# Kernel tuning notes

Measured on AMD Instinct MI355X. Metric: run time of the kernel, lower is better.

Reference implementation:

```python
import jax, jax.numpy as jnp
import numpy as np

NUM_HEADS = 12
HEAD_DIM = 64
EPS = 1e-6


def _layernorm(x, g, b):
    mu = jnp.mean(x, axis=-1, keepdims=True)
    var = jnp.mean(jnp.square(x - mu), axis=-1, keepdims=True)
    return (x - mu) * jax.lax.rsqrt(var + EPS) * g + b


def setup_inputs() -> dict:
    key = jax.random.key(0)
    ks = jax.random.split(key, 8)
    D, DFF = 768, 3072
    s = lambda d: 1.0 / np.sqrt(d)
    return {
        "hidden_states": jax.random.normal(ks[0], (4, 2048, D), jnp.float32),
        "ln1_g": jnp.ones((D,), jnp.float32),
        "ln1_b": jnp.zeros((D,), jnp.float32),
        "w_qkv": jax.random.normal(ks[1], (D, 3 * D), jnp.float32) * s(D),
        "b_qkv": jnp.zeros((3 * D,), jnp.float32),
        "w_attn": jax.random.normal(ks[2], (D, D), jnp.float32) * s(D),
        "b_attn": jnp.zeros((D,), jnp.float32),
        "ln2_g": jnp.ones((D,), jnp.float32),
        "ln2_b": jnp.zeros((D,), jnp.float32),
        "w_in": jax.random.normal(ks[3], (D, DFF), jnp.float32) * s(D),
        "b_in": jnp.zeros((DFF,), jnp.float32),
        "w_out": jax.random.normal(ks[4], (DFF, D), jnp.float32) * s(DFF),
        "b_out": jnp.zeros((D,), jnp.float32),
    }


def reference(hidden_states, ln1_g, ln1_b, w_qkv, b_qkv, w_attn, b_attn,
              ln2_g, ln2_b, w_in, b_in, w_out, b_out):
    B, S, D = hidden_states.shape
    residual = hidden_states
    h = _layernorm(hidden_states, ln1_g, ln1_b)
    # QKV: [B,S,3D] -> [B,S,3,H,hd] -> [3,B,H,S,hd]
    qkv = (h @ w_qkv + b_qkv).reshape(B, S, 3, NUM_HEADS, HEAD_DIM)
    qkv = jnp.transpose(qkv, (2, 0, 3, 1, 4))
    scale = HEAD_DIM ** (-0.5)
    q, k, v = qkv[0] * scale, qkv[1], qkv[2]
    scores = jnp.einsum("bhqd,bhkd->bhqk", q, k)
    attn = jax.nn.softmax(scores, axis=-1)
    o = jnp.einsum("bhqk,bhkd->bhqd", attn, v)
    o = jnp.transpose(o, (0, 2, 1, 3)).reshape(B, S, D)
    h = residual + (o @ w_attn + b_attn)
    residual2 = h
    h2 = _layernorm(h, ln2_g, ln2_b)
    h2 = jax.nn.gelu(h2 @ w_in + b_in, approximate=False)
    h2 = h2 @ w_out + b_out
    return residual2 + h2
```

## Files before the change

kernel.cpp:

```cpp
#include <hip/hip_runtime.h>

typedef __bf16 bf16_t;
typedef bf16_t bf16x8 __attribute__((ext_vector_type(8)));
typedef float f32x4 __attribute__((ext_vector_type(4)));
typedef unsigned short ushortx8 __attribute__((ext_vector_type(8)));
typedef unsigned short ushortx4 __attribute__((ext_vector_type(4)));
typedef short short4v __attribute__((ext_vector_type(4)));

union U8 { ushortx4 h[2]; bf16x8 b; ushortx8 u; };
union SV { bf16_t h[4]; short4v s; };

__device__ __forceinline__ unsigned short f2bf(float f) {
  union { bf16_t h; unsigned short u; } cv;
  cv.h = (bf16_t)f;
  return cv.u;
}

__device__ __forceinline__ void gl_lds16(const unsigned short* g, unsigned short* l) {
  __builtin_amdgcn_global_load_lds((const __attribute__((address_space(1))) void*)g,
                                   (__attribute__((address_space(3))) void*)l,
                                   16, 0, 0);
}

__device__ __forceinline__ float gelu_fast(float v) {
  float v3 = v * v * v;
  float z = -2.30211886f * v - 0.102945f * v3;
  float e = exp2f(z);
  return v * __builtin_amdgcn_rcpf(1.0f + e);
}

__global__ __launch_bounds__(256) void ln_kernel(const float* __restrict__ x,
                                                 const float* __restrict__ g,
                                                 const float* __restrict__ b,
                                                 unsigned short* __restrict__ out) {
  int row = blockIdx.x;
  int t = threadIdx.x;
  const float* xr = x + (size_t)row * 768;
  float v0 = xr[t], v1 = xr[t + 256], v2 = xr[t + 512];
  __shared__ float red[4];
  float s = v0 + v1 + v2;
  for (int o = 32; o > 0; o >>= 1) s += __shfl_down(s, o, 64);
  if ((t & 63) == 0) red[t >> 6] = s;
  __syncthreads();
  float mu = (red[0] + red[1] + red[2] + red[3]) * (1.0f / 768.0f);
  __syncthreads();
  float d0 = v0 - mu, d1 = v1 - mu, d2 = v2 - mu;
  s = d0 * d0 + d1 * d1 + d2 * d2;
  for (int o = 32; o > 0; o >>= 1) s += __shfl_down(s, o, 64);
  if ((t & 63) == 0) red[t >> 6] = s;
  __syncthreads();
  float var = (red[0] + red[1] + red[2] + red[3]) * (1.0f / 768.0f);
  float rs = rsqrtf(var + 1e-6f);
  unsigned short* orow = out + (size_t)row * 768;
  orow[t]       = f2bf(d0 * rs * g[t]       + b[t]);
  orow[t + 256] = f2bf(d1 * rs * g[t + 256] + b[t + 256]);
  orow[t + 512] = f2bf(d2 * rs * g[t + 512] + b[t + 512]);
}

__global__ __launch_bounds__(256) void transpose_all(
    const float* __restrict__ w_qkv, const float* __restrict__ w_attn,
    const float* __restrict__ w_in, const float* __restrict__ w_out,
    unsigned short* __restrict__ wqkvT, unsigned short* __restrict__ wattnT,
    unsigned short* __restrict__ winT, unsigned short* __restrict__ woutT) {
  int id = blockIdx.x;
  const float* W; unsigned short* WT; int K, N, nx, ny;
  if (id < 1728)      { W = w_qkv;  WT = wqkvT;  K = 768;  N = 2304; nx = id % 72; ny = id / 72; }
  else if (id < 2304) { id -= 1728; W = w_attn; WT = wattnT; K = 768;  N = 768;  nx = id % 24; ny = id / 24; }
  else if (id < 4608) { id -= 2304; W = w_in;   WT = winT;   K = 768;  N = 3072; nx = id % 96; ny = id / 96; }
  else                { id -= 4608; W = w_out;  WT = woutT;  K = 3072; N = 768;  nx = id % 24; ny = id / 24; }
  __shared__ float tile[32][33];
  int n0 = nx * 32, k0 = ny * 32;
  int tx = threadIdx.x, ty = threadIdx.y;
  for (int i = 0; i < 4; i++)
    tile[ty + i * 8][tx] = W[(size_t)(k0 + ty + i * 8) * N + n0 + tx];
  __syncthreads();
  for (int i = 0; i < 4; i++)
    WT[(size_t)(n0 + ty + i * 8) * K + k0 + tx] = f2bf(tile[tx][ty + i * 8]);
}

template <int EPI, int TM, int BK>
__device__ __forceinline__ void gemm_body(const unsigned short* __restrict__ A,
                                          const unsigned short* __restrict__ BT,
                                          const float* __restrict__ bias,
                                          const float* resid,
                                          void* out, unsigned short* vt, int os,
                                          int N, int K) {
  constexpr int MI = TM / 32;
  constexpr int ASZ = TM * BK;
  constexpr int BSZ = 128 * BK;
  constexpr int RP = 512 / BK;
  constexpr int NA = TM / (4 * RP);
  constexpr int NB = 128 / (4 * RP);
  constexpr int SM = BK / 8 - 1;
  __shared__ __align__(16) unsigned short smem[2 * (ASZ + BSZ)];

  int t = threadIdx.x;
  int w = t >> 6, lane = t & 63, ln = lane & 15, quad = lane >> 4;
  int wm = w & 1, wn = w >> 1;

  int gx = gridDim.x;
  int nwg = gx * gridDim.y;
  int flat = blockIdx.y * gx + blockIdx.x;
  int nf = (flat & 7) * (nwg >> 3) + (flat >> 3);
  int m0 = (nf / gx) * TM, n0 = (nf % gx) * 128;

  int lrow = lane / (BK / 8);
  int lslot = lane % (BK / 8);
  int scol = ((lslot ^ (lrow & SM)) * 8);

  const unsigned short* gA[NA];
  const unsigned short* gB[NB];
#pragma unroll
  for (int i = 0; i < NA; i++)
    gA[i] = A + (size_t)(m0 + (i * 4 + w) * RP + lrow) * K + scol;
#pragma unroll
  for (int i = 0; i < NB; i++)
    gB[i] = BT + (size_t)(n0 + (i * 4 + w) * RP + lrow) * K + scol;

  auto stage = [&](int buf) {
    unsigned short* Ab = smem + buf * ASZ;
    unsigned short* Bb = smem + 2 * ASZ + buf * BSZ;
#pragma unroll
    for (int i = 0; i < NA; i++) {
      gl_lds16(gA[i], Ab + (i * 4 + w) * 512);
      gA[i] += BK;
    }
#pragma unroll
    for (int i = 0; i < NB; i++) {
      gl_lds16(gB[i], Bb + (i * 4 + w) * 512);
      gB[i] += BK;
    }
  };

  f32x4 acc[MI][4];
  f32x4 zero = {0.f, 0.f, 0.f, 0.f};
  for (int mi = 0; mi < MI; mi++)
    for (int ni = 0; ni < 4; ni++) acc[mi][ni] = zero;

  int nk = K / BK;
  stage(0);
  int cur = 0;
  for (int kt = 0; kt < nk; kt++) {
    __syncthreads();
    if (kt + 1 < nk) stage(cur ^ 1);
    const unsigned short* Ac = smem + cur * ASZ;
    const unsigned short* Bc = smem + 2 * ASZ + cur * BSZ;
#pragma unroll
    for (int ks = 0; ks < BK / 32; ks++) {
      bf16x8 af[MI], bfr[4];
#pragma unroll
      for (int mi = 0; mi < MI; mi++) {
        int r = wm * (TM / 2) + mi * 16 + ln;
        af[mi] = *(const bf16x8*)&Ac[r * BK + (((ks * 4 + quad) ^ (r & SM)) * 8)];
      }
#pragma unroll
      for (int ni = 0; ni < 4; ni++) {
        int r = wn * 64 + ni * 16 + ln;
        bfr[ni] = *(const bf16x8*)&Bc[r * BK + (((ks * 4 + quad) ^ (r & SM)) * 8)];
      }
#pragma unroll
      for (int mi = 0; mi < MI; mi++)
#pragma unroll
        for (int ni = 0; ni < 4; ni++)
          acc[mi][ni] = __builtin_amdgcn_mfma_f32_16x16x32_bf16(af[mi], bfr[ni],
                                                                acc[mi][ni], 0, 0, 0);
    }
    cur ^= 1;
  }

  if (EPI == 2) {
    float* outp = (float*)out;
    for (int mi = 0; mi < MI; mi++) {
      for (int ni = 0; ni < 4; ni++) {
        int col = n0 + wn * 64 + ni * 16 + ln;
        float bv = bias[col];
        for (int r = 0; r < 4; r++) {
          int row = m0 + wm * (TM / 2) + mi * 16 + quad * 4 + r;
          float v = acc[mi][ni][r] + bv;
          v += resid[(size_t)row * N + col];
          outp[(size_t)row * N + col] = v;
        }
      }
    }
  } else {
    __syncthreads();
    unsigned short* Cs16 = smem + w * 1024;
    unsigned short* outp = (unsigned short*)out;
    for (int mi = 0; mi < MI; mi++) {
      for (int ni = 0; ni < 4; ni++) {
        int col = n0 + wn * 64 + ni * 16 + ln;
        float bv = bias[col];
        for (int r = 0; r < 4; r++) {
          float v = acc[mi][ni][r] + bv;
          if (EPI == 0) {
            if (col < 768) v *= 0.18033688f;
          } else {
            v = gelu_fast(v);
          }
          Cs16[(quad * 4 + r) * 64 + ni * 16 + ln] = f2bf(v);
        }
      }
      __syncthreads();
      if (EPI == 0 && n0 >= 1536) {
        int c = n0 - 1536 + wn * 64 + lane;
        int s0 = m0 + wm * (TM / 2) + mi * 16;
        int bb = s0 >> 11, sl = s0 & 2047;
        ushortx8 lo, hi;
        for (int r = 0; r < 8; r++) lo[r] = Cs16[r * 64 + lane];
        for (int r = 0; r < 8; r++) hi[r] = Cs16[(8 + r) * 64 + lane];
        size_t vbase = ((size_t)(bb * 768 + c)) * 2048 + sl;
        *(ushortx8*)&vt[vbase] = lo;
        *(ushortx8*)&vt[vbase + 8] = hi;
      } else {
        int OS = (EPI == 0) ? os : N;
        for (int j = 0; j < 2; j++) {
          int rrow = j * 8 + (lane >> 3);
          int ch = (lane & 7) * 8;
          ushortx8 pv = *(const ushortx8*)&Cs16[rrow * 64 + ch];
          *(ushortx8*)&outp[(size_t)(m0 + wm * (TM / 2) + mi * 16 + rrow) * OS +
                            n0 + wn * 64 + ch] = pv;
        }
      }
      __syncthreads();
    }
  }
}

__global__ __launch_bounds__(256) void gemm_qkv(const unsigned short* A,
    const unsigned short* BT, const float* bias, void* out, unsigned short* vt,
    int N, int K) {
  gemm_body<0, 128, 32>(A, BT, bias, nullptr, out, vt, 1536, N, K);
}
__global__ __launch_bounds__(256) void gemm_attnout(const unsigned short* A,
    const unsigned short* BT, const float* bias, const float* resid, void* out,
    int N, int K) {
  gemm_body<2, 64, 64>(A, BT, bias, resid, out, nullptr, N, N, K);
}
__global__ __launch_bounds__(256) void gemm_ffn1(const unsigned short* A,
    const unsigned short* BT, const float* bias, void* out, int N, int K) {
  gemm_body<1, 128, 32>(A, BT, bias, nullptr, out, nullptr, N, N, K);
}
__global__ __launch_bounds__(256) void gemm_ffn2(const unsigned short* A,
    const unsigned short* BT, const float* bias, const float* resid, void* out,
    int N, int K) {
  gemm_body<2, 64, 64>(A, BT, bias, resid, out, nullptr, N, N, K);
}

__global__ __launch_bounds__(512, 4) void flash_attn(
    const unsigned short* __restrict__ qk, const unsigned short* __restrict__ v_t,
    unsigned short* __restrict__ o) {
  int flat = blockIdx.y * 16 + blockIdx.x;
  int nf = (flat & 7) * 96 + (flat >> 3);
  int qt = nf % 16;
  int bh = nf / 16;
  int b = bh / 12, h = bh % 12;
  int t = threadIdx.x;
  int w = t >> 6, lane = t & 63, ln = lane & 15, quad = lane >> 4;
  int qg = w & 3, kh2 = w >> 2;

  __shared__ __align__(16) unsigned short smem[18432];
  int qrow0 = b * 2048 + qt * 128;
  int qw = qrow0 + qg * 32;

  bf16x8 qf[2][2];
  for (int qi = 0; qi < 2; qi++)
    for (int kh = 0; kh < 2; kh++)
      qf[qi][kh] = *(const bf16x8*)&qk[(size_t)(qw + qi * 16 + ln) * 1536 +
                                      h * 64 + kh * 32 + quad * 8];

  SV ones;
  for (int r = 0; r < 4; r++) ones.h[r] = (bf16_t)1.0f;

  f32x4 zero = {0.f, 0.f, 0.f, 0.f};
  f32x4 o_acc[4][2];
  for (int df = 0; df < 4; df++)
    for (int qi = 0; qi < 2; qi++) o_acc[df][qi] = zero;
  f32x4 l_acc[2] = {zero, zero};

  int sr = t >> 3, sc = (t & 7) * 8;
  ushortx8 kreg = *(const ushortx8*)&qk[(size_t)(b * 2048 + sr) * 1536 + 768 + h * 64 + sc];
  ushortx8 vreg = *(const ushortx8*)&v_t[(size_t)(bh * 64 + sr) * 2048 + sc];

  for (int kt = 0; kt < 32; kt++) {
    unsigned short* Ks = smem + (kt & 1) * 9216;
    unsigned short* Vt = Ks + 4608;
    *(ushortx8*)&Ks[sr * 72 + sc] = kreg;
    *(ushortx8*)&Vt[sr * 72 + sc] = vreg;
    __syncthreads();
    if (kt < 31) {
      int krow0 = b * 2048 + (kt + 1) * 64;
      kreg = *(const ushortx8*)&qk[(size_t)(krow0 + sr) * 1536 + 768 + h * 64 + sc];
      vreg = *(const ushortx8*)&v_t[(size_t)(bh * 64 + sr) * 2048 + (kt + 1) * 64 + sc];
    }

    for (int kf = 0; kf < 2; kf++) {
      int krow = kh2 * 32 + kf * 16;
      f32x4 ST[2] = {zero, zero};
      bf16x8 kA0 = *(const bf16x8*)&Ks[(krow + ln) * 72 + quad * 8];
      bf16x8 kA1 = *(const bf16x8*)&Ks[(krow + ln) * 72 + 32 + quad * 8];
      __builtin_amdgcn_s_setprio(1);
      for (int qi = 0; qi < 2; qi++) {
        ST[qi] = __builtin_amdgcn_mfma_f32_16x16x32_bf16(kA0, qf[qi][0], ST[qi], 0, 0, 0);
        ST[qi] = __builtin_amdgcn_mfma_f32_16x16x32_bf16(kA1, qf[qi][1], ST[qi], 0, 0, 0);
      }
      __builtin_amdgcn_s_setprio(0);
      short4v pT[2];
      for (int qi = 0; qi < 2; qi++) {
        SV pv;
        for (int r = 0; r < 4; r++)
          pv.h[r] = (bf16_t)__builtin_amdgcn_exp2f(ST[qi][r]);
        pT[qi] = pv.s;
      }
      __builtin_amdgcn_s_setprio(1);
      for (int qi = 0; qi < 2; qi++)
        l_acc[qi] = __builtin_amdgcn_mfma_f32_16x16x16bf16_1k(
            ones.s, pT[qi], l_acc[qi], 0, 0, 0);
      for (int df = 0; df < 4; df++) {
        short4v vA = *(const short4v*)&Vt[(df * 16 + ln) * 72 + krow + quad * 4];
        for (int qi = 0; qi < 2; qi++)
          o_acc[df][qi] = __builtin_amdgcn_mfma_f32_16x16x16bf16_1k(
              vA, pT[qi], o_acc[df][qi], 0, 0, 0);
      }
      __builtin_amdgcn_s_setprio(0);
    }
  }

  __syncthreads();
  float* fb = (float*)smem;
  float* fbl = fb + 8320;
  if (kh2 == 1) {
    for (int df = 0; df < 4; df++)
      for (int qi = 0; qi < 2; qi++)
        for (int r = 0; r < 4; r++)
          fb[qg * 2080 + (qi * 16 + ln) * 65 + df * 16 + quad * 4 + r] =
              o_acc[df][qi][r];
    if (quad == 0)
      for (int qi = 0; qi < 2; qi++)
        fbl[qg * 32 + qi * 16 + ln] = l_acc[qi][0];
  }
  __syncthreads();
  float inv[2];
  if (kh2 == 0) {
    for (int qi = 0; qi < 2; qi++) {
      float lt = l_acc[qi][0] + fbl[qg * 32 + qi * 16 + ln];
      inv[qi] = __builtin_amdgcn_rcpf(lt);
    }
    for (int df = 0; df < 4; df++)
      for (int qi = 0; qi < 2; qi++)
        for (int r = 0; r < 4; r++)
          o_acc[df][qi][r] += fb[qg * 2080 + (qi * 16 + ln) * 65 + df * 16 + quad * 4 + r];
  }
  __syncthreads();
  if (kh2 == 0) {
    unsigned short* Osm = smem + qg * 2304;
    for (int qi = 0; qi < 2; qi++)
      for (int df = 0; df < 4; df++)
        for (int r = 0; r < 4; r++)
          Osm[(qi * 16 + ln) * 72 + df * 16 + quad * 4 + r] =
              f2bf(o_acc[df][qi][r] * inv[qi]);
  }
  __syncthreads();
  if (kh2 == 0) {
    unsigned short* Osm = smem + qg * 2304;
    for (int p2 = 0; p2 < 4; p2++) {
      int rr = p2 * 8 + (lane >> 3);
      int ch = (lane & 7) * 8;
      ushortx8 u = *(const ushortx8*)&Osm[rr * 72 + ch];
      *(ushortx8*)&o[(size_t)(qw + rr) * 768 + h * 64 + ch] = u;
    }
  }
}

extern "C" void kernel_launch(void* const* d_in, const int* in_sizes, int n_in,
                              void* d_out, int out_size, void* d_ws, size_t ws_size,
                              hipStream_t stream) {
  const float* hidden = (const float*)d_in[0];
  const float* ln1_g  = (const float*)d_in[1];
  const float* ln1_b  = (const float*)d_in[2];
  const float* w_qkv  = (const float*)d_in[3];
  const float* b_qkv  = (const float*)d_in[4];
  const float* w_attn = (const float*)d_in[5];
  const float* b_attn = (const float*)d_in[6];
  const float* ln2_g  = (const float*)d_in[7];
  const float* ln2_b  = (const float*)d_in[8];
  const float* w_in   = (const float*)d_in[9];
  const float* b_in   = (const float*)d_in[10];
  const float* w_out  = (const float*)d_in[11];
  const float* b_out  = (const float*)d_in[12];
  float* out = (float*)d_out;

  char* ws = (char*)d_ws;
  unsigned short* wqkvT  = (unsigned short*)(ws + 0);
  unsigned short* wattnT = (unsigned short*)(ws + 3538944);
  unsigned short* winT   = (unsigned short*)(ws + 4718592);
  unsigned short* woutT  = (unsigned short*)(ws + 9437184);
  unsigned short* bufX   = (unsigned short*)(ws + 14155776);
  unsigned short* bufBig = (unsigned short*)(ws + 26738688);
  unsigned short* bufQK  = bufBig;
  unsigned short* v_t    = (unsigned short*)(ws + 26738688 + 25165824);

  transpose_all<<<6912, dim3(32, 8), 0, stream>>>(w_qkv, w_attn, w_in, w_out,
                                                  wqkvT, wattnT, winT, woutT);
  ln_kernel<<<8192, 256, 0, stream>>>(hidden, ln1_g, ln1_b, bufX);
  gemm_qkv<<<dim3(18, 64), 256, 0, stream>>>(bufX, wqkvT, b_qkv, (void*)bufQK,
                                             v_t, 2304, 768);
  flash_attn<<<dim3(16, 48), 512, 0, stream>>>(bufQK, v_t, bufX);
  gemm_attnout<<<dim3(6, 128), 256, 0, stream>>>(bufX, wattnT, b_attn, hidden,
                                                 (void*)out, 768, 768);
  ln_kernel<<<8192, 256, 0, stream>>>(out, ln2_g, ln2_b, bufX);
  gemm_ffn1<<<dim3(24, 64), 256, 0, stream>>>(bufX, winT, b_in, (void*)bufBig,
                                              3072, 768);
  gemm_ffn2<<<dim3(6, 128), 256, 0, stream>>>(bufBig, woutT, b_out, out,
                                              (void*)out, 768, 3072);
}
```

Measured before the change: 393.4 us.

## Triple-buffer GEMM k-loop with vmcnt waits and widen attention PV MFMAs

The GEMM body moves from double to triple buffering. Each k-step waits with a partial s_waitcnt vmcnt plus a raw barrier and keeps two stages of loads in flight. All GEMMs are fixed at a 128x128x32 tile, so the attn-out and FFN2 grids halve, which cuts wave count and adds more K work per block. In flash attention, two 16-key fragments are packed into one 8-wide P operand and the 16x16x16 MFMAs are replaced with 16x16x32 ones, with a K row swizzle so the layouts line up. The intent is to hide global-load latency and halve the MFMA instruction count in the PV and row-sum step. The risks are lower occupancy from the larger LDS footprint and fewer blocks for the N=768 GEMMs.

```diff
diff --git a/kernel.cpp b/kernel.cpp
--- a/kernel.cpp
+++ b/kernel.cpp
@@ -7,8 +7,7 @@
 typedef unsigned short ushortx4 __attribute__((ext_vector_type(4)));
 typedef short short4v __attribute__((ext_vector_type(4)));
 
-union U8 { ushortx4 h[2]; bf16x8 b; ushortx8 u; };
-union SV { bf16_t h[4]; short4v s; };
+union UB8 { bf16_t h8[8]; bf16x8 b; };
 
 __device__ __forceinline__ unsigned short f2bf(float f) {
   union { bf16_t h; unsigned short u; } cv;
@@ -78,21 +77,17 @@
     WT[(size_t)(n0 + ty + i * 8) * K + k0 + tx] = f2bf(tile[tx][ty + i * 8]);
 }
 
-template <int EPI, int TM, int BK>
+template <int EPI>
 __device__ __forceinline__ void gemm_body(const unsigned short* __restrict__ A,
                                           const unsigned short* __restrict__ BT,
                                           const float* __restrict__ bias,
                                           const float* resid,
                                           void* out, unsigned short* vt, int os,
                                           int N, int K) {
-  constexpr int MI = TM / 32;
+  constexpr int TM = 128, BK = 32, MI = 4;
   constexpr int ASZ = TM * BK;
-  constexpr int BSZ = 128 * BK;
-  constexpr int RP = 512 / BK;
-  constexpr int NA = TM / (4 * RP);
-  constexpr int NB = 128 / (4 * RP);
-  constexpr int SM = BK / 8 - 1;
-  __shared__ __align__(16) unsigned short smem[2 * (ASZ + BSZ)];
+  constexpr int BUF = ASZ + 128 * BK;
+  __shared__ __align__(16) unsigned short smem[3 * BUF];
 
   int t = threadIdx.x;
   int w = t >> 6, lane = t & 63, ln = lane & 15, quad = lane >> 4;
@@ -104,32 +99,22 @@
   int nf = (flat & 7) * (nwg >> 3) + (flat >> 3);
   int m0 = (nf / gx) * TM, n0 = (nf % gx) * 128;
 
-  int lrow = lane / (BK / 8);
-  int lslot = lane % (BK / 8);
-  int scol = ((lslot ^ (lrow & SM)) * 8);
-
-  const unsigned short* gA[NA];
-  const unsigned short* gB[NB];
-#pragma unroll
-  for (int i = 0; i < NA; i++)
-    gA[i] = A + (size_t)(m0 + (i * 4 + w) * RP + lrow) * K + scol;
-#pragma unroll
-  for (int i = 0; i < NB; i++)
-    gB[i] = BT + (size_t)(n0 + (i * 4 + w) * RP + lrow) * K + scol;
+  int lrow = lane >> 2;
+  int lslot = lane & 3;
+  int scol = (lslot ^ ((lrow >> 1) & 3)) * 8;
+
+  const unsigned short* gA0 = A + (size_t)(m0 + w * 16 + lrow) * K + scol;
+  const unsigned short* gA1 = gA0 + (size_t)64 * K;
+  const unsigned short* gB0 = BT + (size_t)(n0 + w * 16 + lrow) * K + scol;
+  const unsigned short* gB1 = gB0 + (size_t)64 * K;
 
   auto stage = [&](int buf) {
-    unsigned short* Ab = smem + buf * ASZ;
-    unsigned short* Bb = smem + 2 * ASZ + buf * BSZ;
-#pragma unroll
-    for (int i = 0; i < NA; i++) {
-      gl_lds16(gA[i], Ab + (i * 4 + w) * 512);
-      gA[i] += BK;
-    }
-#pragma unroll
-    for (int i = 0; i < NB; i++) {
-      gl_lds16(gB[i], Bb + (i * 4 + w) * 512);
-      gB[i] += BK;
-    }
+    unsigned short* Sb = smem + buf * BUF;
+    gl_lds16(gA0, Sb + w * 512);
+    gl_lds16(gA1, Sb + 2048 + w * 512);
+    gl_lds16(gB0, Sb + ASZ + w * 512);
+    gl_lds16(gB1, Sb + ASZ + 2048 + w * 512);
+    gA0 += BK; gA1 += BK; gB0 += BK; gB1 += BK;
   };
 
   f32x4 acc[MI][4];
@@ -139,33 +124,31 @@
 
   int nk = K / BK;
   stage(0);
+  stage(1);
   int cur = 0;
+  int soff = (quad ^ ((ln >> 1) & 3)) * 8;
   for (int kt = 0; kt < nk; kt++) {
-    __syncthreads();
-    if (kt + 1 < nk) stage(cur ^ 1);
-    const unsigned short* Ac = smem + cur * ASZ;
-    const unsigned short* Bc = smem + 2 * ASZ + cur * BSZ;
-#pragma unroll
-    for (int ks = 0; ks < BK / 32; ks++) {
-      bf16x8 af[MI], bfr[4];
-#pragma unroll
-      for (int mi = 0; mi < MI; mi++) {
-        int r = wm * (TM / 2) + mi * 16 + ln;
-        af[mi] = *(const bf16x8*)&Ac[r * BK + (((ks * 4 + quad) ^ (r & SM)) * 8)];
-      }
-#pragma unroll
-      for (int ni = 0; ni < 4; ni++) {
-        int r = wn * 64 + ni * 16 + ln;
-        bfr[ni] = *(const bf16x8*)&Bc[r * BK + (((ks * 4 + quad) ^ (r & SM)) * 8)];
-      }
-#pragma unroll
-      for (int mi = 0; mi < MI; mi++)
-#pragma unroll
-        for (int ni = 0; ni < 4; ni++)
-          acc[mi][ni] = __builtin_amdgcn_mfma_f32_16x16x32_bf16(af[mi], bfr[ni],
-                                                                acc[mi][ni], 0, 0, 0);
-    }
-    cur ^= 1;
+    if (kt < nk - 1) { asm volatile("s_waitcnt vmcnt(4)" ::: "memory"); }
+    else             { asm volatile("s_waitcnt vmcnt(0)" ::: "memory"); }
+    __builtin_amdgcn_s_barrier();
+    __builtin_amdgcn_sched_barrier(0);
+    int pre = cur + 2; if (pre >= 3) pre -= 3;
+    if (kt + 2 < nk) stage(pre);
+    const unsigned short* Sc = smem + cur * BUF;
+    bf16x8 af[MI], bfr[4];
+#pragma unroll
+    for (int mi = 0; mi < MI; mi++)
+      af[mi] = *(const bf16x8*)&Sc[(wm * 64 + mi * 16 + ln) * 32 + soff];
+#pragma unroll
+    for (int ni = 0; ni < 4; ni++)
+      bfr[ni] = *(const bf16x8*)&Sc[ASZ + (wn * 64 + ni * 16 + ln) * 32 + soff];
+#pragma unroll
+    for (int mi = 0; mi < MI; mi++)
+#pragma unroll
+      for (int ni = 0; ni < 4; ni++)
+        acc[mi][ni] = __builtin_amdgcn_mfma_f32_16x16x32_bf16(af[mi], bfr[ni],
+                                                              acc[mi][ni], 0, 0, 0);
+    cur = cur + 1; if (cur >= 3) cur = 0;
   }
 
   if (EPI == 2) {
@@ -175,7 +158,7 @@
         int col = n0 + wn * 64 + ni * 16 + ln;
         float bv = bias[col];
         for (int r = 0; r < 4; r++) {
-          int row = m0 + wm * (TM / 2) + mi * 16 + quad * 4 + r;
+          int row = m0 + wm * 64 + mi * 16 + quad * 4 + r;
           float v = acc[mi][ni][r] + bv;
           v += resid[(size_t)row * N + col];
           outp[(size_t)row * N + col] = v;
@@ -203,7 +186,7 @@
       __syncthreads();
       if (EPI == 0 && n0 >= 1536) {
         int c = n0 - 1536 + wn * 64 + lane;
-        int s0 = m0 + wm * (TM / 2) + mi * 16;
+        int s0 = m0 + wm * 64 + mi * 16;
         int bb = s0 >> 11, sl = s0 & 2047;
         ushortx8 lo, hi;
         for (int r = 0; r < 8; r++) lo[r] = Cs16[r * 64 + lane];
@@ -217,7 +200,7 @@
           int rrow = j * 8 + (lane >> 3);
           int ch = (lane & 7) * 8;
           ushortx8 pv = *(const ushortx8*)&Cs16[rrow * 64 + ch];
-          *(ushortx8*)&outp[(size_t)(m0 + wm * (TM / 2) + mi * 16 + rrow) * OS +
+          *(ushortx8*)&outp[(size_t)(m0 + wm * 64 + mi * 16 + rrow) * OS +
                             n0 + wn * 64 + ch] = pv;
         }
       }
@@ -229,21 +212,21 @@
 __global__ __launch_bounds__(256) void gemm_qkv(const unsigned short* A,
     const unsigned short* BT, const float* bias, void* out, unsigned short* vt,
     int N, int K) {
-  gemm_body<0, 128, 32>(A, BT, bias, nullptr, out, vt, 1536, N, K);
+  gemm_body<0>(A, BT, bias, nullptr, out, vt, 1536, N, K);
 }
 __global__ __launch_bounds__(256) void gemm_attnout(const unsigned short* A,
     const unsigned short* BT, const float* bias, const float* resid, void* out,
     int N, int K) {
-  gemm_body<2, 64, 64>(A, BT, bias, resid, out, nullptr, N, N, K);
+  gemm_body<2>(A, BT, bias, resid, out, nullptr, N, N, K);
 }
 __global__ __launch_bounds__(256) void gemm_ffn1(const unsigned short* A,
     const unsigned short* BT, const float* bias, void* out, int N, int K) {
-  gemm_body<1, 128, 32>(A, BT, bias, nullptr, out, nullptr, N, N, K);
+  gemm_body<1>(A, BT, bias, nullptr, out, nullptr, N, N, K);
 }
 __global__ __launch_bounds__(256) void gemm_ffn2(const unsigned short* A,
     const unsigned short* BT, const float* bias, const float* resid, void* out,
     int N, int K) {
-  gemm_body<2, 64, 64>(A, BT, bias, resid, out, nullptr, N, N, K);
+  gemm_body<2>(A, BT, bias, resid, out, nullptr, N, N, K);
 }
 
 __global__ __launch_bounds__(512, 4) void flash_attn(
@@ -268,8 +251,9 @@
       qf[qi][kh] = *(const bf16x8*)&qk[(size_t)(qw + qi * 16 + ln) * 1536 +
                                       h * 64 + kh * 32 + quad * 8];
 
-  SV ones;
-  for (int r = 0; r < 4; r++) ones.h[r] = (bf16_t)1.0f;
+  UB8 ones8;
+#pragma unroll
+  for (int r = 0; r < 8; r++) ones8.h8[r] = (bf16_t)1.0f;
 
   f32x4 zero = {0.f, 0.f, 0.f, 0.f};
   f32x4 o_acc[4][2];
@@ -278,13 +262,14 @@
   f32x4 l_acc[2] = {zero, zero};
 
   int sr = t >> 3, sc = (t & 7) * 8;
+  int ssr = (sr & 32) | (((sr >> 2) & 1) << 4) | (((sr >> 3) & 3) << 2) | (sr & 3);
   ushortx8 kreg = *(const ushortx8*)&qk[(size_t)(b * 2048 + sr) * 1536 + 768 + h * 64 + sc];
   ushortx8 vreg = *(const ushortx8*)&v_t[(size_t)(bh * 64 + sr) * 2048 + sc];
 
   for (int kt = 0; kt < 32; kt++) {
     unsigned short* Ks = smem + (kt & 1) * 9216;
     unsigned short* Vt = Ks + 4608;
-    *(ushortx8*)&Ks[sr * 72 + sc] = kreg;
+    *(ushortx8*)&Ks[ssr * 72 + sc] = kreg;
     *(ushortx8*)&Vt[sr * 72 + sc] = vreg;
     __syncthreads();
     if (kt < 31) {
@@ -293,36 +278,40 @@
       vreg = *(const ushortx8*)&v_t[(size_t)(bh * 64 + sr) * 2048 + (kt + 1) * 64 + sc];
     }
 
+    UB8 pb[2];
+#pragma unroll
     for (int kf = 0; kf < 2; kf++) {
       int krow = kh2 * 32 + kf * 16;
       f32x4 ST[2] = {zero, zero};
       bf16x8 kA0 = *(const bf16x8*)&Ks[(krow + ln) * 72 + quad * 8];
       bf16x8 kA1 = *(const bf16x8*)&Ks[(krow + ln) * 72 + 32 + quad * 8];
       __builtin_amdgcn_s_setprio(1);
+#pragma unroll
       for (int qi = 0; qi < 2; qi++) {
         ST[qi] = __builtin_amdgcn_mfma_f32_16x16x32_bf16(kA0, qf[qi][0], ST[qi], 0, 0, 0);
         ST[qi] = __builtin_amdgcn_mfma_f32_16x16x32_bf16(kA1, qf[qi][1], ST[qi], 0, 0, 0);
       }
       __builtin_amdgcn_s_setprio(0);
-      short4v pT[2];
-      for (int qi = 0; qi < 2; qi++) {
-        SV pv;
+#pragma unroll
+      for (int qi = 0; qi < 2; qi++)
+#pragma unroll
         for (int r = 0; r < 4; r++)
-          pv.h[r] = (bf16_t)__builtin_amdgcn_exp2f(ST[qi][r]);
-        pT[qi] = pv.s;
-      }
-      __builtin_amdgcn_s_setprio(1);
+          pb[qi].h8[kf * 4 + r] = (bf16_t)__builtin_amdgcn_exp2f(ST[qi][r]);
+    }
+    __builtin_amdgcn_s_setprio(1);
+#pragma unroll
+    for (int qi = 0; qi < 2; qi++)
+      l_acc[qi] = __builtin_amdgcn_mfma_f32_16x16x32_bf16(ones8.b, pb[qi].b,
+                                                          l_acc[qi], 0, 0, 0);
+#pragma unroll
+    for (int df = 0; df < 4; df++) {
+      bf16x8 vA = *(const bf16x8*)&Vt[(df * 16 + ln) * 72 + kh2 * 32 + quad * 8];
+#pragma unroll
       for (int qi = 0; qi < 2; qi++)
-        l_acc[qi] = __builtin_amdgcn_mfma_f32_16x16x16bf16_1k(
-            ones.s, pT[qi], l_acc[qi], 0, 0, 0);
-      for (int df = 0; df < 4; df++) {
-        short4v vA = *(const short4v*)&Vt[(df * 16 + ln) * 72 + krow + quad * 4];
-        for (int qi = 0; qi < 2; qi++)
-          o_acc[df][qi] = __builtin_amdgcn_mfma_f32_16x16x16bf16_1k(
-              vA, pT[qi], o_acc[df][qi], 0, 0, 0);
-      }
-      __builtin_amdgcn_s_setprio(0);
-    }
+        o_acc[df][qi] = __builtin_amdgcn_mfma_f32_16x16x32_bf16(vA, pb[qi].b,
+                                                                o_acc[df][qi], 0, 0, 0);
+    }
+    __builtin_amdgcn_s_setprio(0);
   }
 
   __syncthreads();
@@ -405,11 +394,11 @@
   gemm_qkv<<<dim3(18, 64), 256, 0, stream>>>(bufX, wqkvT, b_qkv, (void*)bufQK,
                                              v_t, 2304, 768);
   flash_attn<<<dim3(16, 48), 512, 0, stream>>>(bufQK, v_t, bufX);
-  gemm_attnout<<<dim3(6, 128), 256, 0, stream>>>(bufX, wattnT, b_attn, hidden,
-                                                 (void*)out, 768, 768);
+  gemm_attnout<<<dim3(6, 64), 256, 0, stream>>>(bufX, wattnT, b_attn, hidden,
+                                                (void*)out, 768, 768);
   ln_kernel<<<8192, 256, 0, stream>>>(out, ln2_g, ln2_b, bufX);
   gemm_ffn1<<<dim3(24, 64), 256, 0, stream>>>(bufX, winT, b_in, (void*)bufBig,
                                               3072, 768);
-  gemm_ffn2<<<dim3(6, 128), 256, 0, stream>>>(bufBig, woutT, b_out, out,
-                                              (void*)out, 768, 3072);
-}
+  gemm_ffn2<<<dim3(6, 64), 256, 0, stream>>>(bufBig, woutT, b_out, out,
+                                             (void*)out, 768, 3072);
+}
```

New measurement: 382.3 us. -2.8%, faster.
